# Kernel tuning notes

Hardware: AMD Instinct MI355X
Metric: run time of the kernel (lower is better)

Reference implementation:

```python
import jax, jax.numpy as jnp
import numpy as np
from jax import lax

NUM_HEADS = 8
EMBED_DIM = 256
KEY_DIM = EMBED_DIM // NUM_HEADS  # 32


def rotate_every_two(x):
    x1 = x[..., ::2]
    x2 = x[..., 1::2]
    return jnp.stack((-x2, x1), axis=-1).reshape(x.shape)


def theta_shift(x, sin, cos):
    return x * cos + rotate_every_two(x) * sin


def setup_inputs() -> dict:
    key = jax.random.key(0)
    ks = jax.random.split(key, 16)
    b, H, W, E = 16, 64, 64, EMBED_DIM
    kd = KEY_DIM
    gain = 2 ** (-2.5)
    std_proj = gain * (2.0 / (E + E)) ** 0.5  # xavier_normal with gain
    std_out = (2.0 / (E + E)) ** 0.5
    return {
        "x": jax.random.normal(ks[0], (b, H, W, E), jnp.float32),
        "sin": jax.random.normal(ks[1], (H, W, kd), jnp.float32),
        "cos": jax.random.normal(ks[2], (H, W, kd), jnp.float32),
        "mask_h": jax.random.normal(ks[3], (NUM_HEADS, H, H), jnp.float32),
        "mask_w": jax.random.normal(ks[4], (NUM_HEADS, W, W), jnp.float32),
        "q_w": jax.random.normal(ks[5], (E, E), jnp.float32) * std_proj,
        "q_b": jnp.zeros((E,), jnp.float32),
        "k_w": jax.random.normal(ks[6], (E, E), jnp.float32) * std_proj,
        "k_b": jnp.zeros((E,), jnp.float32),
        "v_w": jax.random.normal(ks[7], (E, E), jnp.float32) * std_proj,
        "v_b": jnp.zeros((E,), jnp.float32),
        "lepe_w": jax.random.normal(ks[8], (5, 5, 1, E), jnp.float32) * 0.05,  # HWIO depthwise
        "lepe_b": jnp.zeros((E,), jnp.float32),
        "out_w": jax.random.normal(ks[9], (E, E), jnp.float32) * std_out,
        "out_b": jnp.zeros((E,), jnp.float32),
    }


def reference(x, sin, cos, mask_h, mask_w, q_w, q_b, k_w, k_b, v_w, v_b,
              lepe_w, lepe_b, out_w, out_b):
    b, H, W, E = x.shape
    nH, kd = NUM_HEADS, KEY_DIM
    vd = E // nH
    scaling = kd ** (-0.5)

    q = x @ q_w + q_b                       # [b,H,W,E]
    k = (x @ k_w + k_b) * scaling
    v = x @ v_w + v_b

    # depthwise 5x5 conv (lepe), NHWC
    lepe = lax.conv_general_dilated(
        v, lepe_w, window_strides=(1, 1), padding=[(2, 2), (2, 2)],
        dimension_numbers=("NHWC", "HWIO", "NHWC"), feature_group_count=E) + lepe_b

    q = q.reshape(b, H, W, nH, kd)
    k = k.reshape(b, H, W, nH, kd)
    v = v.reshape(b, H, W, nH, vd)

    sin_b = sin[:, :, None, :]              # [H,W,1,kd]
    cos_b = cos[:, :, None, :]
    qr = theta_shift(q, sin_b, cos_b)       # [b,H,W,nH,kd]
    kr = theta_shift(k, sin_b, cos_b)

    # width-wise attention: scores [b,H,nH,W,W]
    qk_w = jnp.einsum("bhqnd,bhknd->bhnqk", qr, kr)
    attn_w = jax.nn.softmax(qk_w + mask_w[None, None], axis=-1)
    v1 = jnp.einsum("bhnqk,bhknd->bhqnd", attn_w, v)  # [b,H,W,nH,vd]

    # height-wise attention: scores [b,W,nH,H,H]
    qk_h = jnp.einsum("bqwnd,bkwnd->bwnqk", qr, kr)
    attn_h = jax.nn.softmax(qk_h + mask_h[None, None], axis=-1)
    out = jnp.einsum("bwnqk,bkwnd->bqwnd", attn_h, v1)  # [b,H,W,nH,vd]

    out = out.reshape(b, H, W, E) + lepe
    return out @ out_w + out_b
```

## Files before the change

### kernel.cpp

```cpp
#include <hip/hip_runtime.h>

typedef unsigned short u16;
typedef __attribute__((ext_vector_type(4))) float f32x4;
typedef __attribute__((ext_vector_type(8))) short bf16x8;
typedef __attribute__((ext_vector_type(8))) u16 u16x8;
typedef __attribute__((ext_vector_type(4))) u16 u16x4v;

#define DI __device__ __forceinline__

DI u16 f2bf(float f) {
  unsigned int x = __float_as_uint(f);
  unsigned int r = (x + 0x7fffu + ((x >> 16) & 1u)) >> 16;
  return (u16)r;
}
DI float bf2f(u16 u) { return __uint_as_float(((unsigned int)u) << 16); }

__global__ __launch_bounds__(256) void pack_kernel(
    const float* __restrict__ qw, const float* __restrict__ qb,
    const float* __restrict__ kw, const float* __restrict__ kb,
    const float* __restrict__ vw, const float* __restrict__ vb,
    const float* __restrict__ ow,
    u16* __restrict__ wqkvT, float* __restrict__ bias, u16* __restrict__ owT)
{
  const int r = blockIdx.x;
  const int t = threadIdx.x;
  if (r < 768) {
    const int p = r >> 8, c = r & 255;
    const float* wsrc = p == 0 ? qw : (p == 1 ? kw : vw);
    const float sc = (p == 1) ? 0.17677669529663687f : 1.0f;
    wqkvT[r * 256 + t] = f2bf(wsrc[t * 256 + c] * sc);
    if (t == 0) {
      const float* bs = p == 0 ? qb : (p == 1 ? kb : vb);
      bias[r] = bs[c] * sc;
    }
  } else {
    const int c = r - 768;
    owT[c * 256 + t] = f2bf(ow[t * 256 + c]);
  }
}

__global__ __launch_bounds__(256) void convert_kernel(
    const float* __restrict__ x, u16* __restrict__ xb)
{
  const int idx = blockIdx.x * 256 + threadIdx.x;
  const int tile = idx >> 12;
  const int within = idx & 4095;
  const int r = within >> 5;
  const int bc = (within & 31) << 4;
  const int sbc = bc ^ ((r & 7) << 4);
  const int row = (tile << 7) + r;
  const float* sp = x + row * 256 + (sbc >> 1);
  const float4 a = *reinterpret_cast<const float4*>(sp);
  const float4 b = *reinterpret_cast<const float4*>(sp + 4);
  u16x8 o;
  o[0] = f2bf(a.x); o[1] = f2bf(a.y); o[2] = f2bf(a.z); o[3] = f2bf(a.w);
  o[4] = f2bf(b.x); o[5] = f2bf(b.y); o[6] = f2bf(b.z); o[7] = f2bf(b.w);
  *reinterpret_cast<u16x8*>(xb + (idx << 3)) = o;
}

__global__ __launch_bounds__(256, 2) void qkv_gemm_kernel(
    const u16* __restrict__ xb, const u16* __restrict__ wT, const float* __restrict__ bias,
    const float* __restrict__ sinp, const float* __restrict__ cosp,
    u16* __restrict__ qr, u16* __restrict__ kr, u16* __restrict__ v)
{
  __shared__ u16 As[32768];
  __shared__ float Tr[4][1024];
  const int t = threadIdx.x;
  const int wave = t >> 6, lane = t & 63;
  const int g = lane >> 4, lr = lane & 15;
  const int wr = wave >> 1, wc = wave & 1;
  const int m0 = blockIdx.x * 128;

  {
    const u16* src = xb + (size_t)blockIdx.x * 32768;
    auto gsrc = (const __attribute__((address_space(1))) u16*)src;
    auto lds = (__attribute__((address_space(3))) u16*)As;
#pragma unroll
    for (int i = 0; i < 16; ++i) {
      const int o = wave * 8192 + i * 512;
      __builtin_amdgcn_global_load_lds(
          (const __attribute__((address_space(1))) void*)(gsrc + o + lane * 8),
          (__attribute__((address_space(3))) void*)(lds + o), 16, 0, 0);
    }
  }
  __syncthreads();

  const char* Ab = (const char*)As;
  float* Trw = Tr[wave];
  const int tl = (lane >> 3);
  const int cg8 = (lane & 7) * 8;

  for (int cg = 0; cg < 6; ++cg) {
    const int c0 = cg * 128;
    f32x4 acc[4][4];
#pragma unroll
    for (int i = 0; i < 4; ++i)
#pragma unroll
      for (int j = 0; j < 4; ++j) acc[i][j] = (f32x4){0.f, 0.f, 0.f, 0.f};

#pragma unroll
    for (int ks = 0; ks < 8; ++ks) {
      bf16x8 af[4], bfr[4];
#pragma unroll
      for (int mt = 0; mt < 4; ++mt) {
        const int rr = wr * 64 + mt * 16 + lr;
        const int cb = (ks * 64 + g * 16) ^ ((rr & 7) << 4);
        af[mt] = *reinterpret_cast<const bf16x8*>(Ab + rr * 512 + cb);
      }
#pragma unroll
      for (int nt = 0; nt < 4; ++nt)
        bfr[nt] = *reinterpret_cast<const bf16x8*>(wT + (c0 + wc * 64 + nt * 16 + lr) * 256 + ks * 32 + g * 8);
#pragma unroll
      for (int mt = 0; mt < 4; ++mt)
#pragma unroll
        for (int nt = 0; nt < 4; ++nt)
          acc[mt][nt] = __builtin_amdgcn_mfma_f32_16x16x32_bf16(af[mt], bfr[nt], acc[mt][nt], 0, 0, 0);
    }

    const int colb = c0 + wc * 64;
    const int proj = colb >> 8;
    u16* dst = proj == 0 ? qr : (proj == 1 ? kr : v);
    const int e0 = (colb & 255) + cg8;

    float bcv[4];
#pragma unroll
    for (int nt = 0; nt < 4; ++nt) bcv[nt] = bias[colb + nt * 16 + lr];

#pragma unroll
    for (int mt = 0; mt < 4; ++mt) {
#pragma unroll
      for (int nt = 0; nt < 4; ++nt)
#pragma unroll
        for (int j = 0; j < 4; ++j)
          Trw[(g * 4 + j) * 64 + ((nt * 16 + lr) ^ (g << 4))] = acc[mt][nt][j] + bcv[nt];
      asm volatile("s_waitcnt lgkmcnt(0)" ::: "memory");
#pragma unroll
      for (int r2 = 0; r2 < 2; ++r2) {
        const int row = tl + 8 * r2;
        const int rb = row * 64 + (cg8 ^ ((row >> 2) << 4));
        const float4 v0 = *reinterpret_cast<const float4*>(Trw + rb);
        const float4 v1 = *reinterpret_cast<const float4*>(Trw + rb + 4);
        const int tok = m0 + wr * 64 + mt * 16 + row;
        float r0, r1, r2v, r3, r4, r5, r6, r7;
        if (proj < 2) {
          const int pos = tok & 4095;
          const int d0 = cg8 & 31;
          const float* sp2 = sinp + pos * 32 + d0;
          const float* cp2 = cosp + pos * 32 + d0;
          const float4 s0 = *reinterpret_cast<const float4*>(sp2);
          const float4 s1 = *reinterpret_cast<const float4*>(sp2 + 4);
          const float4 cA = *reinterpret_cast<const float4*>(cp2);
          const float4 cB = *reinterpret_cast<const float4*>(cp2 + 4);
          r0  = v0.x * cA.x - v0.y * s0.x;
          r1  = v0.y * cA.y + v0.x * s0.y;
          r2v = v0.z * cA.z - v0.w * s0.z;
          r3  = v0.w * cA.w + v0.z * s0.w;
          r4  = v1.x * cB.x - v1.y * s1.x;
          r5  = v1.y * cB.y + v1.x * s1.y;
          r6  = v1.z * cB.z - v1.w * s1.z;
          r7  = v1.w * cB.w + v1.z * s1.w;
        } else {
          r0 = v0.x; r1 = v0.y; r2v = v0.z; r3 = v0.w;
          r4 = v1.x; r5 = v1.y; r6 = v1.z; r7 = v1.w;
        }
        u16x8 o;
        o[0] = f2bf(r0);  o[1] = f2bf(r1);  o[2] = f2bf(r2v); o[3] = f2bf(r3);
        o[4] = f2bf(r4);  o[5] = f2bf(r5);  o[6] = f2bf(r6);  o[7] = f2bf(r7);
        *reinterpret_cast<u16x8*>(dst + tok * 256 + e0) = o;
      }
      asm volatile("s_waitcnt lgkmcnt(0)" ::: "memory");
    }
  }
}

__global__ __launch_bounds__(256, 2) void attn_kernel(
    const u16* __restrict__ qr, const u16* __restrict__ kr, const u16* __restrict__ vsrc,
    const float* __restrict__ mask, u16* __restrict__ dst, const int mode)
{
  __shared__ u16 Pbuf[4][64][72];
  __shared__ u16 Vs[64][260];
  const int t = threadIdx.x;
  const int wave = t >> 6, lane = t & 63;
  const int g = lane >> 4, lr = lane & 15;
  const int b = blockIdx.x >> 6, o = blockIdx.x & 63;
  const int base = (mode == 0) ? (b * 4096 + o * 64) * 256 : (b * 4096 + o) * 256;
  const int ts = (mode == 0) ? 256 : 16384;

#pragma unroll
  for (int i = 0; i < 16; ++i) {
    const int idx = t + 256 * i;
    const int tok = idx >> 6, c4 = (idx & 63) << 2;
    *reinterpret_cast<u16x4v*>(&Vs[tok][c4]) =
        *reinterpret_cast<const u16x4v*>(vsrc + base + tok * ts + c4);
  }
  __syncthreads();

  for (int hh = 0; hh < 2; ++hh) {
    const int n = wave * 2 + hh;
    bf16x8 qf[4], kf[4];
#pragma unroll
    for (int mt = 0; mt < 4; ++mt) {
      qf[mt] = *reinterpret_cast<const bf16x8*>(qr + base + (mt * 16 + lr) * ts + n * 32 + g * 8);
      kf[mt] = *reinterpret_cast<const bf16x8*>(kr + base + (mt * 16 + lr) * ts + n * 32 + g * 8);
    }
    const f32x4 zero = (f32x4){0.f, 0.f, 0.f, 0.f};
    f32x4 s[4][4];
#pragma unroll
    for (int mt = 0; mt < 4; ++mt)
#pragma unroll
      for (int nt = 0; nt < 4; ++nt)
        s[mt][nt] = __builtin_amdgcn_mfma_f32_16x16x32_bf16(qf[mt], kf[nt], zero, 0, 0, 0);

    const float* mp = mask + n * 4096;
#pragma unroll
    for (int mt = 0; mt < 4; ++mt) {
#pragma unroll
      for (int j = 0; j < 4; ++j) {
        const int r = mt * 16 + g * 4 + j;
#pragma unroll
        for (int nt = 0; nt < 4; ++nt)
          s[mt][nt][j] += mp[r * 64 + nt * 16 + lr];
        float m = fmaxf(fmaxf(s[mt][0][j], s[mt][1][j]), fmaxf(s[mt][2][j], s[mt][3][j]));
        m = fmaxf(m, __shfl_xor(m, 1));
        m = fmaxf(m, __shfl_xor(m, 2));
        m = fmaxf(m, __shfl_xor(m, 4));
        m = fmaxf(m, __shfl_xor(m, 8));
        float sum = 0.f;
#pragma unroll
        for (int nt = 0; nt < 4; ++nt) {
          const float p = __expf(s[mt][nt][j] - m);
          s[mt][nt][j] = p;
          sum += p;
        }
        sum += __shfl_xor(sum, 1);
        sum += __shfl_xor(sum, 2);
        sum += __shfl_xor(sum, 4);
        sum += __shfl_xor(sum, 8);
        const float rs = 1.f / sum;
#pragma unroll
        for (int nt = 0; nt < 4; ++nt)
          Pbuf[wave][r][nt * 16 + lr] = f2bf(s[mt][nt][j] * rs);
      }
    }
    __syncthreads();

    f32x4 oacc[4][2];
#pragma unroll
    for (int mt = 0; mt < 4; ++mt)
#pragma unroll
      for (int nd = 0; nd < 2; ++nd) oacc[mt][nd] = zero;

#pragma unroll
    for (int kt = 0; kt < 2; ++kt) {
      bf16x8 pa[4];
#pragma unroll
      for (int mt = 0; mt < 4; ++mt)
        pa[mt] = *reinterpret_cast<const bf16x8*>(&Pbuf[wave][mt * 16 + lr][kt * 32 + g * 8]);
#pragma unroll
      for (int nd = 0; nd < 2; ++nd) {
        const int dcol = n * 32 + nd * 16 + lr;
        bf16x8 vb;
#pragma unroll
        for (int j2 = 0; j2 < 8; ++j2)
          vb[j2] = (short)Vs[kt * 32 + g * 8 + j2][dcol];
#pragma unroll
        for (int mt = 0; mt < 4; ++mt)
          oacc[mt][nd] = __builtin_amdgcn_mfma_f32_16x16x32_bf16(pa[mt], vb, oacc[mt][nd], 0, 0, 0);
      }
    }
#pragma unroll
    for (int mt = 0; mt < 4; ++mt)
#pragma unroll
      for (int nd = 0; nd < 2; ++nd)
#pragma unroll
        for (int j = 0; j < 4; ++j)
          dst[base + (mt * 16 + g * 4 + j) * ts + n * 32 + nd * 16 + lr] = f2bf(oacc[mt][nd][j]);
    __syncthreads();
  }
}

__global__ __launch_bounds__(256) void lepe_kernel(
    const u16* __restrict__ v, const float* __restrict__ cw, const float* __restrict__ cb,
    u16* __restrict__ lepe)
{
  const int t = threadIdx.x;
  const int cg = t & 31, pg = t >> 5;
  const int c0 = cg * 8;
  const int rowi = blockIdx.x >> 1;
  const int w0 = (blockIdx.x & 1) * 32 + pg * 4;
  const int h = rowi & 63;

  float acc[4][8];
#pragma unroll
  for (int p = 0; p < 4; ++p)
#pragma unroll
    for (int j = 0; j < 8; ++j) acc[p][j] = 0.f;

#pragma unroll
  for (int dy = 0; dy < 5; ++dy) {
    const int hh = h + dy - 2;
    if ((unsigned)hh >= 64u) continue;
    const u16* vrow = v + (size_t)(rowi + dy - 2) * 64 * 256 + c0;
    float fin[8][8];
#pragma unroll
    for (int i = 0; i < 8; ++i) {
      const int ww = w0 - 2 + i;
      if ((unsigned)ww < 64u) {
        const u16x8 val = *reinterpret_cast<const u16x8*>(vrow + ww * 256);
#pragma unroll
        for (int j = 0; j < 8; ++j) fin[i][j] = bf2f(val[j]);
      } else {
#pragma unroll
        for (int j = 0; j < 8; ++j) fin[i][j] = 0.f;
      }
    }
#pragma unroll
    for (int dx = 0; dx < 5; ++dx) {
      const float* wp = cw + (dy * 5 + dx) * 256 + c0;
      const float4 wA = *reinterpret_cast<const float4*>(wp);
      const float4 wB = *reinterpret_cast<const float4*>(wp + 4);
      const float wv[8] = {wA.x, wA.y, wA.z, wA.w, wB.x, wB.y, wB.z, wB.w};
#pragma unroll
      for (int p = 0; p < 4; ++p)
#pragma unroll
        for (int j = 0; j < 8; ++j)
          acc[p][j] += fin[p + dx][j] * wv[j];
    }
  }

#pragma unroll
  for (int p = 0; p < 4; ++p) {
    u16x8 r;
#pragma unroll
    for (int j = 0; j < 8; ++j) r[j] = f2bf(acc[p][j] + cb[c0 + j]);
    *reinterpret_cast<u16x8*>(lepe + ((size_t)rowi * 64 + w0 + p) * 256 + c0) = r;
  }
}

__global__ __launch_bounds__(256, 2) void out_gemm_kernel(
    const u16* __restrict__ ao, const u16* __restrict__ lep, const u16* __restrict__ owT,
    const float* __restrict__ ob, float* __restrict__ out)
{
  __shared__ u16 As[32768];
  const int t = threadIdx.x;
  const int wave = t >> 6, lane = t & 63;
  const int g = lane >> 4, lr = lane & 15;
  const int wr = wave >> 1, wc = wave & 1;
  const int m0 = blockIdx.x * 128;

  char* Abw = (char*)As;
#pragma unroll
  for (int i = 0; i < 16; ++i) {
    const int idx = t + 256 * i;
    const int r = idx >> 5;
    const int bc = (idx & 31) << 4;
    const int off = (m0 + r) * 256 + (bc >> 1);
    const u16x8 a = *reinterpret_cast<const u16x8*>(ao + off);
    const u16x8 l = *reinterpret_cast<const u16x8*>(lep + off);
    u16x8 s;
#pragma unroll
    for (int j = 0; j < 8; ++j) s[j] = f2bf(bf2f(a[j]) + bf2f(l[j]));
    *reinterpret_cast<u16x8*>(Abw + r * 512 + (bc ^ ((r & 7) << 4))) = s;
  }
  __syncthreads();

  const char* Ab = (const char*)As;
  for (int cg = 0; cg < 2; ++cg) {
    const int c0 = cg * 128;
    f32x4 acc[4][4];
#pragma unroll
    for (int i = 0; i < 4; ++i)
#pragma unroll
      for (int j = 0; j < 4; ++j) acc[i][j] = (f32x4){0.f, 0.f, 0.f, 0.f};

#pragma unroll
    for (int ks = 0; ks < 8; ++ks) {
      bf16x8 af[4], bfr[4];
#pragma unroll
      for (int mt = 0; mt < 4; ++mt) {
        const int rr = wr * 64 + mt * 16 + lr;
        const int cb = (ks * 64 + g * 16) ^ ((rr & 7) << 4);
        af[mt] = *reinterpret_cast<const bf16x8*>(Ab + rr * 512 + cb);
      }
#pragma unroll
      for (int nt = 0; nt < 4; ++nt)
        bfr[nt] = *reinterpret_cast<const bf16x8*>(owT + (c0 + wc * 64 + nt * 16 + lr) * 256 + ks * 32 + g * 8);
#pragma unroll
      for (int mt = 0; mt < 4; ++mt)
#pragma unroll
        for (int nt = 0; nt < 4; ++nt)
          acc[mt][nt] = __builtin_amdgcn_mfma_f32_16x16x32_bf16(af[mt], bfr[nt], acc[mt][nt], 0, 0, 0);
    }

#pragma unroll
    for (int mt = 0; mt < 4; ++mt) {
#pragma unroll
      for (int nt = 0; nt < 4; ++nt) {
        const int col = c0 + wc * 64 + nt * 16 + lr;
        const float bc2 = ob[col];
#pragma unroll
        for (int j = 0; j < 4; ++j) {
          const int tok = m0 + wr * 64 + mt * 16 + g * 4 + j;
          out[tok * 256 + col] = acc[mt][nt][j] + bc2;
        }
      }
    }
  }
}

extern "C" void kernel_launch(void* const* d_in, const int* in_sizes, int n_in,
                              void* d_out, int out_size, void* d_ws, size_t ws_size,
                              hipStream_t stream)
{
  const float* x      = (const float*)d_in[0];
  const float* sinp   = (const float*)d_in[1];
  const float* cosp   = (const float*)d_in[2];
  const float* mask_h = (const float*)d_in[3];
  const float* mask_w = (const float*)d_in[4];
  const float* q_w    = (const float*)d_in[5];
  const float* q_b    = (const float*)d_in[6];
  const float* k_w    = (const float*)d_in[7];
  const float* k_b    = (const float*)d_in[8];
  const float* v_w    = (const float*)d_in[9];
  const float* v_b    = (const float*)d_in[10];
  const float* lepe_w = (const float*)d_in[11];
  const float* lepe_b = (const float*)d_in[12];
  const float* out_w  = (const float*)d_in[13];
  const float* out_b  = (const float*)d_in[14];

  unsigned char* ws = (unsigned char*)d_ws;
  const size_t SZ = 33554432;
  u16* qr    = (u16*)(ws);
  u16* kr    = (u16*)(ws + SZ);
  u16* vv    = (u16*)(ws + 2 * SZ);
  u16* v1    = (u16*)(ws + 3 * SZ);
  u16* xb    = (u16*)(ws + 4 * SZ);
  u16* lepe  = (u16*)(ws + 4 * SZ);
  u16* wqkvT = (u16*)(ws + 5 * SZ);
  u16* owT   = (u16*)(ws + 5 * SZ + 393216);
  float* bias = (float*)(ws + 5 * SZ + 393216 + 131072);
  u16* attn_out = vv;

  pack_kernel<<<1024, 256, 0, stream>>>(q_w, q_b, k_w, k_b, v_w, v_b, out_w, wqkvT, bias, owT);
  convert_kernel<<<8192, 256, 0, stream>>>(x, xb);
  qkv_gemm_kernel<<<512, 256, 0, stream>>>(xb, wqkvT, bias, sinp, cosp, qr, kr, vv);
  lepe_kernel<<<2048, 256, 0, stream>>>(vv, lepe_w, lepe_b, lepe);
  attn_kernel<<<1024, 256, 0, stream>>>(qr, kr, vv, mask_w, v1, 0);
  attn_kernel<<<1024, 256, 0, stream>>>(qr, kr, v1, mask_h, attn_out, 1);
  out_gemm_kernel<<<512, 256, 0, stream>>>(attn_out, lepe, owT, out_b, (float*)d_out);
}
```

Before: 281.8 us.

## Fuse fp32-to-bf16 conversion into QKV GEMM, shrink GEMM tiles, transpose V in LDS

The separate convert kernel is removed, and the QKV GEMM now reads fp32 x directly, converting it to bf16 while writing LDS. Both GEMMs move from 128-row to 64-row tiles with 1024 blocks and launch bounds of 6 blocks per CU, which raises occupancy but cuts data reuse per block. The attention kernel stores V transposed and swizzled so B fragments come from one vector LDS read instead of eight scalar gathers. It also drops two per-iteration block barriers, relying on per-wave Pbuf ownership.

```diff
diff --git a/kernel.cpp b/kernel.cpp
--- a/kernel.cpp
+++ b/kernel.cpp
@@ -39,136 +39,113 @@
   }
 }
 
-__global__ __launch_bounds__(256) void convert_kernel(
-    const float* __restrict__ x, u16* __restrict__ xb)
-{
-  const int idx = blockIdx.x * 256 + threadIdx.x;
-  const int tile = idx >> 12;
-  const int within = idx & 4095;
-  const int r = within >> 5;
-  const int bc = (within & 31) << 4;
-  const int sbc = bc ^ ((r & 7) << 4);
-  const int row = (tile << 7) + r;
-  const float* sp = x + row * 256 + (sbc >> 1);
-  const float4 a = *reinterpret_cast<const float4*>(sp);
-  const float4 b = *reinterpret_cast<const float4*>(sp + 4);
-  u16x8 o;
-  o[0] = f2bf(a.x); o[1] = f2bf(a.y); o[2] = f2bf(a.z); o[3] = f2bf(a.w);
-  o[4] = f2bf(b.x); o[5] = f2bf(b.y); o[6] = f2bf(b.z); o[7] = f2bf(b.w);
-  *reinterpret_cast<u16x8*>(xb + (idx << 3)) = o;
-}
-
-__global__ __launch_bounds__(256, 2) void qkv_gemm_kernel(
-    const u16* __restrict__ xb, const u16* __restrict__ wT, const float* __restrict__ bias,
+__global__ __launch_bounds__(256, 6) void qkv_gemm_kernel(
+    const float* __restrict__ x, const u16* __restrict__ wT, const float* __restrict__ bias,
     const float* __restrict__ sinp, const float* __restrict__ cosp,
     u16* __restrict__ qr, u16* __restrict__ kr, u16* __restrict__ v)
 {
-  __shared__ u16 As[32768];
-  __shared__ float Tr[4][1024];
+  __shared__ u16 As[16384];
+  __shared__ float Tr[4][2][576];
   const int t = threadIdx.x;
   const int wave = t >> 6, lane = t & 63;
   const int g = lane >> 4, lr = lane & 15;
-  const int wr = wave >> 1, wc = wave & 1;
-  const int m0 = blockIdx.x * 128;
+  const int m0 = blockIdx.x * 64;
 
   {
-    const u16* src = xb + (size_t)blockIdx.x * 32768;
-    auto gsrc = (const __attribute__((address_space(1))) u16*)src;
-    auto lds = (__attribute__((address_space(3))) u16*)As;
+    char* Abw = (char*)As;
 #pragma unroll
     for (int i = 0; i < 16; ++i) {
-      const int o = wave * 8192 + i * 512;
-      __builtin_amdgcn_global_load_lds(
-          (const __attribute__((address_space(1))) void*)(gsrc + o + lane * 8),
-          (__attribute__((address_space(3))) void*)(lds + o), 16, 0, 0);
+      const int c = t + 256 * i;
+      const int row = c >> 6, cf = c & 63;
+      const float4 xv = *reinterpret_cast<const float4*>(x + (m0 + row) * 256 + cf * 4);
+      u16x4v bv;
+      bv.x = f2bf(xv.x); bv.y = f2bf(xv.y); bv.z = f2bf(xv.z); bv.w = f2bf(xv.w);
+      *reinterpret_cast<u16x4v*>(Abw + row * 512 + ((cf * 8) ^ ((row & 7) << 4))) = bv;
     }
   }
   __syncthreads();
 
   const char* Ab = (const char*)As;
-  float* Trw = Tr[wave];
-  const int tl = (lane >> 3);
-  const int cg8 = (lane & 7) * 8;
+  const int tl8 = lane >> 2;
+  const int c8 = (lane & 3) * 8;
 
   for (int cg = 0; cg < 6; ++cg) {
     const int c0 = cg * 128;
-    f32x4 acc[4][4];
+    f32x4 acc[4][2];
 #pragma unroll
     for (int i = 0; i < 4; ++i)
 #pragma unroll
-      for (int j = 0; j < 4; ++j) acc[i][j] = (f32x4){0.f, 0.f, 0.f, 0.f};
+      for (int j = 0; j < 2; ++j) acc[i][j] = (f32x4){0.f, 0.f, 0.f, 0.f};
 
 #pragma unroll
     for (int ks = 0; ks < 8; ++ks) {
-      bf16x8 af[4], bfr[4];
+      bf16x8 af[4], bfr[2];
 #pragma unroll
       for (int mt = 0; mt < 4; ++mt) {
-        const int rr = wr * 64 + mt * 16 + lr;
+        const int rr = mt * 16 + lr;
         const int cb = (ks * 64 + g * 16) ^ ((rr & 7) << 4);
         af[mt] = *reinterpret_cast<const bf16x8*>(Ab + rr * 512 + cb);
       }
 #pragma unroll
-      for (int nt = 0; nt < 4; ++nt)
-        bfr[nt] = *reinterpret_cast<const bf16x8*>(wT + (c0 + wc * 64 + nt * 16 + lr) * 256 + ks * 32 + g * 8);
+      for (int nt = 0; nt < 2; ++nt)
+        bfr[nt] = *reinterpret_cast<const bf16x8*>(wT + (c0 + wave * 32 + nt * 16 + lr) * 256 + ks * 32 + g * 8);
 #pragma unroll
       for (int mt = 0; mt < 4; ++mt)
 #pragma unroll
-        for (int nt = 0; nt < 4; ++nt)
+        for (int nt = 0; nt < 2; ++nt)
           acc[mt][nt] = __builtin_amdgcn_mfma_f32_16x16x32_bf16(af[mt], bfr[nt], acc[mt][nt], 0, 0, 0);
     }
 
-    const int colb = c0 + wc * 64;
+    const int colb = c0 + wave * 32;
     const int proj = colb >> 8;
     u16* dst = proj == 0 ? qr : (proj == 1 ? kr : v);
-    const int e0 = (colb & 255) + cg8;
-
-    float bcv[4];
-#pragma unroll
-    for (int nt = 0; nt < 4; ++nt) bcv[nt] = bias[colb + nt * 16 + lr];
+    const int e0 = (colb & 255) + c8;
+
+    float bcv[2];
+#pragma unroll
+    for (int nt = 0; nt < 2; ++nt) bcv[nt] = bias[colb + nt * 16 + lr];
 
 #pragma unroll
     for (int mt = 0; mt < 4; ++mt) {
-#pragma unroll
-      for (int nt = 0; nt < 4; ++nt)
+      float* Trb = Tr[wave][mt & 1];
+#pragma unroll
+      for (int nt = 0; nt < 2; ++nt)
 #pragma unroll
         for (int j = 0; j < 4; ++j)
-          Trw[(g * 4 + j) * 64 + ((nt * 16 + lr) ^ (g << 4))] = acc[mt][nt][j] + bcv[nt];
+          Trb[(g * 4 + j) * 36 + nt * 16 + lr] = acc[mt][nt][j] + bcv[nt];
       asm volatile("s_waitcnt lgkmcnt(0)" ::: "memory");
-#pragma unroll
-      for (int r2 = 0; r2 < 2; ++r2) {
-        const int row = tl + 8 * r2;
-        const int rb = row * 64 + (cg8 ^ ((row >> 2) << 4));
-        const float4 v0 = *reinterpret_cast<const float4*>(Trw + rb);
-        const float4 v1 = *reinterpret_cast<const float4*>(Trw + rb + 4);
-        const int tok = m0 + wr * 64 + mt * 16 + row;
-        float r0, r1, r2v, r3, r4, r5, r6, r7;
-        if (proj < 2) {
-          const int pos = tok & 4095;
-          const int d0 = cg8 & 31;
-          const float* sp2 = sinp + pos * 32 + d0;
-          const float* cp2 = cosp + pos * 32 + d0;
+      const int rb = tl8 * 36 + c8;
+      const int tok = m0 + mt * 16 + tl8;
+      u16x8 o;
+      if (proj < 2) {
+        const int pos = tok & 4095;
+        const float* sp2 = sinp + pos * 32 + c8;
+        const float* cp2 = cosp + pos * 32 + c8;
+        {
+          const float4 v0 = *reinterpret_cast<const float4*>(Trb + rb);
           const float4 s0 = *reinterpret_cast<const float4*>(sp2);
+          const float4 cA = *reinterpret_cast<const float4*>(cp2);
+          o[0] = f2bf(v0.x * cA.x - v0.y * s0.x);
+          o[1] = f2bf(v0.y * cA.y + v0.x * s0.y);
+          o[2] = f2bf(v0.z * cA.z - v0.w * s0.z);
+          o[3] = f2bf(v0.w * cA.w + v0.z * s0.w);
+        }
+        {
+          const float4 v1 = *reinterpret_cast<const float4*>(Trb + rb + 4);
           const float4 s1 = *reinterpret_cast<const float4*>(sp2 + 4);
-          const float4 cA = *reinterpret_cast<const float4*>(cp2);
           const float4 cB = *reinterpret_cast<const float4*>(cp2 + 4);
-          r0  = v0.x * cA.x - v0.y * s0.x;
-          r1  = v0.y * cA.y + v0.x * s0.y;
-          r2v = v0.z * cA.z - v0.w * s0.z;
-          r3  = v0.w * cA.w + v0.z * s0.w;
-          r4  = v1.x * cB.x - v1.y * s1.x;
-          r5  = v1.y * cB.y + v1.x * s1.y;
-          r6  = v1.z * cB.z - v1.w * s1.z;
-          r7  = v1.w * cB.w + v1.z * s1.w;
-        } else {
-          r0 = v0.x; r1 = v0.y; r2v = v0.z; r3 = v0.w;
-          r4 = v1.x; r5 = v1.y; r6 = v1.z; r7 = v1.w;
+          o[4] = f2bf(v1.x * cB.x - v1.y * s1.x);
+          o[5] = f2bf(v1.y * cB.y + v1.x * s1.y);
+          o[6] = f2bf(v1.z * cB.z - v1.w * s1.z);
+          o[7] = f2bf(v1.w * cB.w + v1.z * s1.w);
         }
-        u16x8 o;
-        o[0] = f2bf(r0);  o[1] = f2bf(r1);  o[2] = f2bf(r2v); o[3] = f2bf(r3);
-        o[4] = f2bf(r4);  o[5] = f2bf(r5);  o[6] = f2bf(r6);  o[7] = f2bf(r7);
-        *reinterpret_cast<u16x8*>(dst + tok * 256 + e0) = o;
-      }
-      asm volatile("s_waitcnt lgkmcnt(0)" ::: "memory");
+      } else {
+        const float4 v0 = *reinterpret_cast<const float4*>(Trb + rb);
+        const float4 v1 = *reinterpret_cast<const float4*>(Trb + rb + 4);
+        o[0] = f2bf(v0.x); o[1] = f2bf(v0.y); o[2] = f2bf(v0.z); o[3] = f2bf(v0.w);
+        o[4] = f2bf(v1.x); o[5] = f2bf(v1.y); o[6] = f2bf(v1.z); o[7] = f2bf(v1.w);
+      }
+      *reinterpret_cast<u16x8*>(dst + tok * 256 + e0) = o;
     }
   }
 }
@@ -178,7 +155,7 @@
     const float* __restrict__ mask, u16* __restrict__ dst, const int mode)
 {
   __shared__ u16 Pbuf[4][64][72];
-  __shared__ u16 Vs[64][260];
+  __shared__ u16 Vt[256][80];
   const int t = threadIdx.x;
   const int wave = t >> 6, lane = t & 63;
   const int g = lane >> 4, lr = lane & 15;
@@ -187,11 +164,13 @@
   const int ts = (mode == 0) ? 256 : 16384;
 
 #pragma unroll
-  for (int i = 0; i < 16; ++i) {
-    const int idx = t + 256 * i;
-    const int tok = idx >> 6, c4 = (idx & 63) << 2;
-    *reinterpret_cast<u16x4v*>(&Vs[tok][c4]) =
-        *reinterpret_cast<const u16x4v*>(vsrc + base + tok * ts + c4);
+  for (int i = 0; i < 8; ++i) {
+    const int c = t + 256 * i;
+    const int tok = c >> 5, ch = c & 31;
+    const u16x8 val = *reinterpret_cast<const u16x8*>(vsrc + base + tok * ts + ch * 8);
+    const int tc = tok ^ ((ch & 7) * 8);
+#pragma unroll
+    for (int j = 0; j < 8; ++j) Vt[ch * 8 + j][tc] = val[j];
   }
   __syncthreads();
 
@@ -242,7 +221,6 @@
           Pbuf[wave][r][nt * 16 + lr] = f2bf(s[mt][nt][j] * rs);
       }
     }
-    __syncthreads();
 
     f32x4 oacc[4][2];
 #pragma unroll
@@ -259,10 +237,8 @@
 #pragma unroll
       for (int nd = 0; nd < 2; ++nd) {
         const int dcol = n * 32 + nd * 16 + lr;
-        bf16x8 vb;
-#pragma unroll
-        for (int j2 = 0; j2 < 8; ++j2)
-          vb[j2] = (short)Vs[kt * 32 + g * 8 + j2][dcol];
+        const bf16x8 vb = *reinterpret_cast<const bf16x8*>(
+            &Vt[dcol][(kt * 32 + g * 8) ^ (((dcol >> 3) & 7) * 8)]);
 #pragma unroll
         for (int mt = 0; mt < 4; ++mt)
           oacc[mt][nd] = __builtin_amdgcn_mfma_f32_16x16x32_bf16(pa[mt], vb, oacc[mt][nd], 0, 0, 0);
@@ -275,7 +251,6 @@
 #pragma unroll
         for (int j = 0; j < 4; ++j)
           dst[base + (mt * 16 + g * 4 + j) * ts + n * 32 + nd * 16 + lr] = f2bf(oacc[mt][nd][j]);
-    __syncthreads();
   }
 }
 
@@ -337,70 +312,68 @@
   }
 }
 
-__global__ __launch_bounds__(256, 2) void out_gemm_kernel(
+__global__ __launch_bounds__(256, 6) void out_gemm_kernel(
     const u16* __restrict__ ao, const u16* __restrict__ lep, const u16* __restrict__ owT,
     const float* __restrict__ ob, float* __restrict__ out)
 {
-  __shared__ u16 As[32768];
+  __shared__ u16 As[16384];
   const int t = threadIdx.x;
   const int wave = t >> 6, lane = t & 63;
   const int g = lane >> 4, lr = lane & 15;
-  const int wr = wave >> 1, wc = wave & 1;
-  const int m0 = blockIdx.x * 128;
+  const int m0 = blockIdx.x * 64;
 
   char* Abw = (char*)As;
 #pragma unroll
-  for (int i = 0; i < 16; ++i) {
-    const int idx = t + 256 * i;
-    const int r = idx >> 5;
-    const int bc = (idx & 31) << 4;
-    const int off = (m0 + r) * 256 + (bc >> 1);
+  for (int i = 0; i < 8; ++i) {
+    const int c = t + 256 * i;
+    const int row = c >> 5, bc = (c & 31) << 4;
+    const int off = (m0 + row) * 256 + (c & 31) * 8;
     const u16x8 a = *reinterpret_cast<const u16x8*>(ao + off);
     const u16x8 l = *reinterpret_cast<const u16x8*>(lep + off);
     u16x8 s;
 #pragma unroll
     for (int j = 0; j < 8; ++j) s[j] = f2bf(bf2f(a[j]) + bf2f(l[j]));
-    *reinterpret_cast<u16x8*>(Abw + r * 512 + (bc ^ ((r & 7) << 4))) = s;
+    *reinterpret_cast<u16x8*>(Abw + row * 512 + (bc ^ ((row & 7) << 4))) = s;
   }
   __syncthreads();
 
   const char* Ab = (const char*)As;
   for (int cg = 0; cg < 2; ++cg) {
-    const int c0 = cg * 128;
-    f32x4 acc[4][4];
+    const int c0 = cg * 128 + wave * 32;
+    f32x4 acc[4][2];
 #pragma unroll
     for (int i = 0; i < 4; ++i)
 #pragma unroll
-      for (int j = 0; j < 4; ++j) acc[i][j] = (f32x4){0.f, 0.f, 0.f, 0.f};
+      for (int j = 0; j < 2; ++j) acc[i][j] = (f32x4){0.f, 0.f, 0.f, 0.f};
 
 #pragma unroll
     for (int ks = 0; ks < 8; ++ks) {
-      bf16x8 af[4], bfr[4];
+      bf16x8 af[4], bfr[2];
 #pragma unroll
       for (int mt = 0; mt < 4; ++mt) {
-        const int rr = wr * 64 + mt * 16 + lr;
+        const int rr = mt * 16 + lr;
         const int cb = (ks * 64 + g * 16) ^ ((rr & 7) << 4);
         af[mt] = *reinterpret_cast<const bf16x8*>(Ab + rr * 512 + cb);
       }
 #pragma unroll
-      for (int nt = 0; nt < 4; ++nt)
-        bfr[nt] = *reinterpret_cast<const bf16x8*>(owT + (c0 + wc * 64 + nt * 16 + lr) * 256 + ks * 32 + g * 8);
+      for (int nt = 0; nt < 2; ++nt)
+        bfr[nt] = *reinterpret_cast<const bf16x8*>(owT + (c0 + nt * 16 + lr) * 256 + ks * 32 + g * 8);
 #pragma unroll
       for (int mt = 0; mt < 4; ++mt)
 #pragma unroll
-        for (int nt = 0; nt < 4; ++nt)
+        for (int nt = 0; nt < 2; ++nt)
           acc[mt][nt] = __builtin_amdgcn_mfma_f32_16x16x32_bf16(af[mt], bfr[nt], acc[mt][nt], 0, 0, 0);
     }
 
 #pragma unroll
     for (int mt = 0; mt < 4; ++mt) {
 #pragma unroll
-      for (int nt = 0; nt < 4; ++nt) {
-        const int col = c0 + wc * 64 + nt * 16 + lr;
+      for (int nt = 0; nt < 2; ++nt) {
+        const int col = c0 + nt * 16 + lr;
         const float bc2 = ob[col];
 #pragma unroll
         for (int j = 0; j < 4; ++j) {
-          const int tok = m0 + wr * 64 + mt * 16 + g * 4 + j;
+          const int tok = m0 + mt * 16 + g * 4 + j;
           out[tok * 256 + col] = acc[mt][nt][j] + bc2;
         }
       }
@@ -434,7 +407,6 @@
   u16* kr    = (u16*)(ws + SZ);
   u16* vv    = (u16*)(ws + 2 * SZ);
   u16* v1    = (u16*)(ws + 3 * SZ);
-  u16* xb    = (u16*)(ws + 4 * SZ);
   u16* lepe  = (u16*)(ws + 4 * SZ);
   u16* wqkvT = (u16*)(ws + 5 * SZ);
   u16* owT   = (u16*)(ws + 5 * SZ + 393216);
@@ -442,10 +414,9 @@
   u16* attn_out = vv;
 
   pack_kernel<<<1024, 256, 0, stream>>>(q_w, q_b, k_w, k_b, v_w, v_b, out_w, wqkvT, bias, owT);
-  convert_kernel<<<8192, 256, 0, stream>>>(x, xb);
-  qkv_gemm_kernel<<<512, 256, 0, stream>>>(xb, wqkvT, bias, sinp, cosp, qr, kr, vv);
+  qkv_gemm_kernel<<<1024, 256, 0, stream>>>(x, wqkvT, bias, sinp, cosp, qr, kr, vv);
   lepe_kernel<<<2048, 256, 0, stream>>>(vv, lepe_w, lepe_b, lepe);
   attn_kernel<<<1024, 256, 0, stream>>>(qr, kr, vv, mask_w, v1, 0);
   attn_kernel<<<1024, 256, 0, stream>>>(qr, kr, v1, mask_h, attn_out, 1);
-  out_gemm_kernel<<<512, 256, 0, stream>>>(attn_out, lepe, owT, out_b, (float*)d_out);
-}
+  out_gemm_kernel<<<1024, 256, 0, stream>>>(attn_out, lepe, owT, out_b, (float*)d_out);
+}
```

New measurement: 276.7 us. No clear change (-1.8%).
